# Kernel tuning notes

Measured on AMD Instinct MI355X. Metric: run time of the kernel, lower is better.

## Reference

```python
import jax, jax.numpy as jnp
import numpy as np


def setup_inputs() -> dict:
    key = jax.random.key(0)
    ks = jax.random.split(key, 6)
    L, B, A, I, H = 512, 64, 256, 256, 512
    scale = 1.0 / np.sqrt(H)
    return {
        "action_features": jax.random.normal(ks[0], (L, B, A), dtype=jnp.float32),
        "input_feature": jax.random.normal(ks[1], (B, I), dtype=jnp.float32),
        "h0": jnp.zeros((B, H), dtype=jnp.float32),
        "c0": jnp.zeros((B, H), dtype=jnp.float32),
        "W_ih": jax.random.normal(ks[2], (4 * H, I + A), dtype=jnp.float32) * scale,
        "W_hh": jax.random.normal(ks[3], (4 * H, H), dtype=jnp.float32) * scale,
        "b_ih": jax.random.normal(ks[4], (4 * H,), dtype=jnp.float32) * scale,
        "b_hh": jax.random.normal(ks[5], (4 * H,), dtype=jnp.float32) * scale,
    }


def reference(action_features, input_feature, h0, c0, W_ih, W_hh, b_ih, b_hh):
    # action_features: [L, B, A] (time-major); input_feature: [B, I]
    H = h0.shape[-1]
    L = action_features.shape[0]
    # Precompute the input-side projection for all timesteps at once:
    # x_t = concat([input_feature, a_t]) -> x_t @ W_ih.T + b_ih
    # Split W_ih into the input_feature part and the action part.
    I = input_feature.shape[-1]
    W_i, W_a = W_ih[:, :I], W_ih[:, I:]
    # [B, 4H] contribution from the static input_feature (same every step)
    static_gates = input_feature @ W_i.T + b_ih + b_hh
    # [L, B, 4H] contribution from the per-step action features
    act_gates = jnp.einsum("lba,ga->lbg", action_features, W_a)

    def step(carry, g_t):
        h, c = carry
        gates = g_t + static_gates + h @ W_hh.T  # [B, 4H]
        i, f, g, o = jnp.split(gates, 4, axis=-1)
        i = jax.nn.sigmoid(i)
        f = jax.nn.sigmoid(f)
        g = jnp.tanh(g)
        o = jax.nn.sigmoid(o)
        c_new = f * c + i * g
        h_new = o * jnp.tanh(c_new)
        return (h_new, c_new), h_new

    (h_n, c_n), hs = jax.lax.scan(step, (h0, c0), act_gates)
    return hs, h_n, c_n
```

## Files before the change

### kernel.cpp

```cpp
#include <hip/hip_runtime.h>
#include <hip/hip_bf16.h>


#define NWG     64
#define LSTEPS  512
#define BATCH   64
#define HDIM    512
#define ADIM    256
#define GDIM    2048
#define KTOT    768
#define LBH     (LSTEPS*BATCH*HDIM)

typedef __attribute__((ext_vector_type(4))) float f32x4;
typedef __attribute__((ext_vector_type(8))) short s16x8;

__device__ __forceinline__ unsigned short f2bf(float f){
  unsigned u = __builtin_bit_cast(unsigned, f);
  u = (u + 0x7fffu + ((u >> 16) & 1u)) >> 16;
  return (unsigned short)u;
}
__device__ __forceinline__ float sigm(float x){ return 1.f / (1.f + __expf(-x)); }
__device__ __forceinline__ float ftanh(float x){ return 1.f - 2.f / (__expf(2.f*x) + 1.f); }


__global__ void cvt_act(const float* __restrict__ in, unsigned short* __restrict__ ob, int n8){
  int i = blockIdx.x * blockDim.x + threadIdx.x;
  if (i >= n8) return;
  const float4* p = (const float4*)in + (size_t)i * 2;
  float4 a = p[0], b = p[1];
  int4 o;
  o.x = (int)((unsigned)f2bf(a.x) | ((unsigned)f2bf(a.y) << 16));
  o.y = (int)((unsigned)f2bf(a.z) | ((unsigned)f2bf(a.w) << 16));
  o.z = (int)((unsigned)f2bf(b.x) | ((unsigned)f2bf(b.y) << 16));
  o.w = (int)((unsigned)f2bf(b.z) | ((unsigned)f2bf(b.w) << 16));
  ((int4*)ob)[i] = o;
}

__global__ void static_gates_k(const float* __restrict__ inp, const float* __restrict__ Wih,
                               const float* __restrict__ bih, const float* __restrict__ bhh,
                               float* __restrict__ statg){
  int g = blockIdx.x;
  int b = threadIdx.x;
  const float4* w = (const float4*)(Wih + (size_t)g * 512);
  const float4* x = (const float4*)(inp + (size_t)b * 256);
  float acc = 0.f;
#pragma unroll 8
  for (int i = 0; i < 64; ++i){
    float4 wv = w[i], xv = x[i];
    acc += wv.x*xv.x + wv.y*xv.y + wv.z*xv.z + wv.w*xv.w;
  }
  statg[b*GDIM + g] = acc + bih[g] + bhh[g];
}

__global__ void init_h(const float* __restrict__ h0, unsigned int* __restrict__ hbuf32){
  int i = blockIdx.x * blockDim.x + threadIdx.x;
  if (i < BATCH*256){
    unsigned lo = f2bf(h0[2*i]), hi = f2bf(h0[2*i+1]);
    hbuf32[BATCH*256 + i] = lo | (hi << 16);
  }
}


__global__ __launch_bounds__(256, 1) void lstm_persistent(
    const unsigned short* __restrict__ act_bf,
    const float*          __restrict__ statg,
    const float*          __restrict__ Whh,
    const float*          __restrict__ Wih,
    const float*          __restrict__ c0,
    float*                __restrict__ out,
    unsigned int*         __restrict__ hbuf32,
    unsigned int*         __restrict__ done)
{
  __shared__ short Albuf[64 * KTOT];
  __shared__ float gbuf[64 * 36];

  const int tid  = threadIdx.x;
  const int wgk  = blockIdx.x;
  const int lane = tid & 63;
  const int wid  = tid >> 6;
  const int wm   = wid & 1;
  const int wn   = wid >> 1;
  const int kgrp = (lane >> 4) * 8;

  const int cl   = wn*16 + (lane & 15);
  const int grow = (cl >> 3)*512 + wgk*8 + (cl & 7);
  s16x8 bw[24];
#pragma unroll
  for (int kk = 0; kk < 16; ++kk){
    s16x8 v;
    const int kb = kk*32 + kgrp;
#pragma unroll
    for (int e = 0; e < 8; ++e)
      v[e] = (short)f2bf(Whh[(size_t)grow*512 + kb + e]);
    bw[kk] = v;
  }
#pragma unroll
  for (int kk = 16; kk < 24; ++kk){
    s16x8 v;
    const int kb = kk*32 + kgrp;
#pragma unroll
    for (int e = 0; e < 8; ++e)
      v[e] = (short)f2bf(Wih[(size_t)grow*512 + (kb - 256) + e]);
    bw[kk] = v;
  }

  const int b_cu = tid >> 2;
  const int u0   = (tid & 3) * 2;
  const int j0   = wgk*8 + u0;
  float stat2[2][4], cr[2];
#pragma unroll
  for (int pi = 0; pi < 2; ++pi){
    const int j = j0 + pi;
#pragma unroll
    for (int g4 = 0; g4 < 4; ++g4)
      stat2[pi][g4] = statg[b_cu*GDIM + g4*512 + j];
    cr[pi] = c0[b_cu*HDIM + j];
  }

  for (int t = 0; t < LSTEPS; ++t){
    {
      const unsigned short* asrc = act_bf + (size_t)t * (BATCH*ADIM);
#pragma unroll
      for (int it = 0; it < 8; ++it){
        const int idx = it*256 + tid;
        const int r = idx >> 5, ch = idx & 31;
        int4 v = *(const int4*)(asrc + r*ADIM + ch*8);
        *(int4*)(&Albuf[r*KTOT + 512 + ((ch ^ (r & 7)) * 8)]) = v;
      }
    }
    if (t > 0){
      while (__hip_atomic_load(&done[t-1], __ATOMIC_RELAXED, __HIP_MEMORY_SCOPE_AGENT) < NWG){}
      __builtin_amdgcn_fence(__ATOMIC_ACQUIRE, "agent");
    }
    {
      const int4* hp = (const int4*)(hbuf32 + ((t+1) & 1) * (BATCH*256));
#pragma unroll
      for (int it = 0; it < 16; ++it){
        const int idx = it*256 + tid;
        const int r = idx >> 6, ch = idx & 63;
        int4 v = hp[r*64 + ch];
        *(int4*)(&Albuf[r*KTOT + ((ch ^ (r & 7)) * 8)]) = v;
      }
    }
    __syncthreads();

    f32x4 acc[2];
#pragma unroll
    for (int m = 0; m < 2; ++m){
      f32x4 a = {0.f, 0.f, 0.f, 0.f};
      const int r  = wm*32 + m*16 + (lane & 15);
      const short* arow = &Albuf[r * KTOT];
      const int sw = (r & 7) * 8;
#pragma unroll
      for (int kk = 0; kk < 24; ++kk){
        const int col = (kk*32 + kgrp) ^ sw;
        s16x8 af = *(const s16x8*)(arow + col);
        a = __builtin_amdgcn_mfma_f32_16x16x32_bf16(af, bw[kk], a, 0, 0, 0);
      }
      acc[m] = a;
    }
#pragma unroll
    for (int m = 0; m < 2; ++m){
      const int base_b = wm*32 + m*16 + ((lane >> 4) * 4);
#pragma unroll
      for (int r4 = 0; r4 < 4; ++r4)
        gbuf[(base_b + r4)*36 + cl] = acc[m][r4];
    }
    __syncthreads();

    {
      const float* gb = &gbuf[b_cu*36];
      float hv[2];
#pragma unroll
      for (int pi = 0; pi < 2; ++pi){
        const int u = u0 + pi;
        float iv = gb[u]      + stat2[pi][0];
        float fv = gb[8 + u]  + stat2[pi][1];
        float gv = gb[16 + u] + stat2[pi][2];
        float ov = gb[24 + u] + stat2[pi][3];
        iv = sigm(iv); fv = sigm(fv); gv = ftanh(gv); ov = sigm(ov);
        float c = fv * cr[pi] + iv * gv;
        cr[pi] = c;
        hv[pi] = ov * ftanh(c);
      }
      float2 h2; h2.x = hv[0]; h2.y = hv[1];
      *(float2*)&out[((size_t)t*BATCH + b_cu)*HDIM + j0] = h2;
      unsigned pk = (unsigned)f2bf(hv[0]) | ((unsigned)f2bf(hv[1]) << 16);
      __hip_atomic_store(&hbuf32[(t & 1)*(BATCH*256) + b_cu*256 + (j0 >> 1)], pk,
                         __ATOMIC_RELAXED, __HIP_MEMORY_SCOPE_AGENT);
      if (t == LSTEPS-1){
        float2 c2; c2.x = cr[0]; c2.y = cr[1];
        *(float2*)&out[LBH + b_cu*HDIM + j0] = h2;
        *(float2*)&out[LBH + BATCH*HDIM + b_cu*HDIM + j0] = c2;
      }
    }
    __syncthreads();
    if (tid == 0)
      __hip_atomic_fetch_add(&done[t], 1u, __ATOMIC_RELAXED, __HIP_MEMORY_SCOPE_AGENT);
  }
}


extern "C" void kernel_launch(void* const* d_in, const int* in_sizes, int n_in,
                              void* d_out, int out_size, void* d_ws, size_t ws_size,
                              hipStream_t stream){
  const float* act = (const float*)d_in[0];
  const float* inp = (const float*)d_in[1];
  const float* h0  = (const float*)d_in[2];
  const float* c0  = (const float*)d_in[3];
  const float* Wih = (const float*)d_in[4];
  const float* Whh = (const float*)d_in[5];
  const float* bih = (const float*)d_in[6];
  const float* bhh = (const float*)d_in[7];
  float* out = (float*)d_out;

  char* ws = (char*)d_ws;
  unsigned short* act_bf = (unsigned short*)ws;
  unsigned int*   hbuf32 = (unsigned int*)(ws + 16777216);
  float*          statg  = (float*)(ws + 16777216 + 131072);
  unsigned int*   done   = (unsigned int*)(ws + 16777216 + 131072 + 524288);

  hipMemsetAsync(done, 0, LSTEPS * sizeof(unsigned int), stream);
  cvt_act<<<4096, 256, 0, stream>>>(act, act_bf, (LSTEPS*BATCH*ADIM)/8);
  static_gates_k<<<GDIM, 64, 0, stream>>>(inp, Wih, bih, bhh, statg);
  init_h<<<64, 256, 0, stream>>>(h0, hbuf32);
  lstm_persistent<<<NWG, 256, 0, stream>>>(act_bf, statg, Whh, Wih, c0, out, hbuf32, done);
}
```

Baseline: 2.428 ms.

## Restructure persistent LSTM step: weights as A operand, per-WG flags, prefetch actions

Swaps the MFMA operand roles so the weights sit in the A operand, arranged so that each lane's accumulator holds all four gates (i, f, g, o) for one hidden unit. The gate math can then run straight from registers, and the gbuf shared-memory round trip plus one barrier are gone. The grid barrier changes from an atomic counter fetch_add per step to per-workgroup flag stores in a ring of 8 slots, polled by a whole wavefront with __all. The next step's action tile is now loaded into LDS after the h publish, overlapping it with the wait, and h is published as 64-bit atomic stores by one wave. The risk is memory ordering: the acquire fence was removed and replaced with relaxed loads plus an s_waitcnt, and h values are read back from LDS after the barrier.

```diff
diff --git a/kernel.cpp b/kernel.cpp
--- a/kernel.cpp
+++ b/kernel.cpp
@@ -10,9 +10,11 @@
 #define GDIM    2048
 #define KTOT    768
 #define LBH     (LSTEPS*BATCH*HDIM)
+#define HWORDS  (BATCH*256)
 
 typedef __attribute__((ext_vector_type(4))) float f32x4;
 typedef __attribute__((ext_vector_type(8))) short s16x8;
+typedef unsigned long long u64t;
 
 __device__ __forceinline__ unsigned short f2bf(float f){
   unsigned u = __builtin_bit_cast(unsigned, f);
@@ -54,9 +56,9 @@
 
 __global__ void init_h(const float* __restrict__ h0, unsigned int* __restrict__ hbuf32){
   int i = blockIdx.x * blockDim.x + threadIdx.x;
-  if (i < BATCH*256){
+  if (i < HWORDS){
     unsigned lo = f2bf(h0[2*i]), hi = f2bf(h0[2*i+1]);
-    hbuf32[BATCH*256 + i] = lo | (hi << 16);
+    hbuf32[HWORDS + i] = lo | (hi << 16);
   }
 }
 
@@ -72,19 +74,19 @@
     unsigned int*         __restrict__ done)
 {
   __shared__ short Albuf[64 * KTOT];
-  __shared__ float gbuf[64 * 36];
-
-  const int tid  = threadIdx.x;
-  const int wgk  = blockIdx.x;
-  const int lane = tid & 63;
-  const int wid  = tid >> 6;
-  const int wm   = wid & 1;
-  const int wn   = wid >> 1;
-  const int kgrp = (lane >> 4) * 8;
-
-  const int cl   = wn*16 + (lane & 15);
-  const int grow = (cl >> 3)*512 + wgk*8 + (cl & 7);
-  s16x8 bw[24];
+  __shared__ float hb[64 * 9];
+
+  const int tid   = threadIdx.x;
+  const int wgk   = blockIdx.x;
+  const int lane  = tid & 63;
+  const int wid   = tid >> 6;
+  const int m     = wid & 1;
+  const int npair = wid >> 1;
+  const int kgrp  = (lane >> 4) * 8;
+
+  const int rit  = lane & 15;
+  const int grow = (rit & 3)*512 + wgk*8 + m*4 + (rit >> 2);
+  s16x8 aw[24];
 #pragma unroll
   for (int kk = 0; kk < 16; ++kk){
     s16x8 v;
@@ -92,7 +94,7 @@
 #pragma unroll
     for (int e = 0; e < 8; ++e)
       v[e] = (short)f2bf(Whh[(size_t)grow*512 + kb + e]);
-    bw[kk] = v;
+    aw[kk] = v;
   }
 #pragma unroll
   for (int kk = 16; kk < 24; ++kk){
@@ -101,25 +103,126 @@
 #pragma unroll
     for (int e = 0; e < 8; ++e)
       v[e] = (short)f2bf(Wih[(size_t)grow*512 + (kb - 256) + e]);
-    bw[kk] = v;
-  }
-
-  const int b_cu = tid >> 2;
-  const int u0   = (tid & 3) * 2;
-  const int j0   = wgk*8 + u0;
-  float stat2[2][4], cr[2];
-#pragma unroll
-  for (int pi = 0; pi < 2; ++pi){
-    const int j = j0 + pi;
-#pragma unroll
-    for (int g4 = 0; g4 < 4; ++g4)
-      stat2[pi][g4] = statg[b_cu*GDIM + g4*512 + j];
-    cr[pi] = c0[b_cu*HDIM + j];
+    aw[kk] = v;
+  }
+
+  const int bA = (npair*2)*16 + (lane & 15);
+  const int bB = bA + 16;
+  const int j  = wgk*8 + m*4 + (lane >> 4);
+  const int uloc = m*4 + (lane >> 4);
+  float stat[2][4], cr[2];
+#pragma unroll
+  for (int g4 = 0; g4 < 4; ++g4){
+    stat[0][g4] = statg[bA*GDIM + g4*512 + j];
+    stat[1][g4] = statg[bB*GDIM + g4*512 + j];
+  }
+  cr[0] = c0[bA*HDIM + j];
+  cr[1] = c0[bB*HDIM + j];
+
+  const int r0  = bA;
+  const int sw0 = (r0 & 7) * 8;
+
+  {
+    const unsigned short* asrc = act_bf;
+#pragma unroll
+    for (int it = 0; it < 8; ++it){
+      const int idx = it*256 + tid;
+      const int r = idx >> 5, ch = idx & 31;
+      int4 v = *(const int4*)(asrc + r*ADIM + ch*8);
+      *(int4*)(&Albuf[r*KTOT + 512 + ((ch ^ (r & 7)) * 8)]) = v;
+    }
   }
 
   for (int t = 0; t < LSTEPS; ++t){
-    {
-      const unsigned short* asrc = act_bf + (size_t)t * (BATCH*ADIM);
+    if (t > 0){
+      unsigned v;
+      const unsigned* fl = &done[((t-1) & 7)*64 + lane];
+      do {
+        v = __hip_atomic_load(fl, __ATOMIC_RELAXED, __HIP_MEMORY_SCOPE_AGENT);
+      } while (!__all(v == (unsigned)t));
+    }
+    {
+      const u64t* hsrc = (const u64t*)(hbuf32 + ((t+1) & 1) * HWORDS);
+#pragma unroll
+      for (int it = 0; it < 16; ++it){
+        const int idx = it*256 + tid;
+        const int r = idx >> 6, ch = idx & 63;
+        u64t a = __hip_atomic_load(hsrc + r*128 + ch*2,     __ATOMIC_RELAXED, __HIP_MEMORY_SCOPE_AGENT);
+        u64t b = __hip_atomic_load(hsrc + r*128 + ch*2 + 1, __ATOMIC_RELAXED, __HIP_MEMORY_SCOPE_AGENT);
+        int4 v;
+        v.x = (int)(unsigned)(a & 0xffffffffull);
+        v.y = (int)(unsigned)(a >> 32);
+        v.z = (int)(unsigned)(b & 0xffffffffull);
+        v.w = (int)(unsigned)(b >> 32);
+        *(int4*)(&Albuf[r*KTOT + ((ch ^ (r & 7)) * 8)]) = v;
+      }
+    }
+    __syncthreads();
+
+    f32x4 acc0 = {0.f,0.f,0.f,0.f}, acc1 = {0.f,0.f,0.f,0.f};
+    {
+      const short* arow0 = &Albuf[r0 * KTOT];
+      const short* arow1 = &Albuf[(r0+16) * KTOT];
+#pragma unroll
+      for (int kk = 0; kk < 24; ++kk){
+        const int col = (kk*32 + kgrp) ^ sw0;
+        s16x8 b0 = *(const s16x8*)(arow0 + col);
+        s16x8 b1 = *(const s16x8*)(arow1 + col);
+        acc0 = __builtin_amdgcn_mfma_f32_16x16x32_bf16(aw[kk], b0, acc0, 0, 0, 0);
+        acc1 = __builtin_amdgcn_mfma_f32_16x16x32_bf16(aw[kk], b1, acc1, 0, 0, 0);
+      }
+    }
+
+    float hv[2];
+    {
+      float iv = sigm(acc0[0] + stat[0][0]);
+      float fv = sigm(acc0[1] + stat[0][1]);
+      float gv = ftanh(acc0[2] + stat[0][2]);
+      float ov = sigm(acc0[3] + stat[0][3]);
+      float c = fv * cr[0] + iv * gv;
+      cr[0] = c; hv[0] = ov * ftanh(c);
+      iv = sigm(acc1[0] + stat[1][0]);
+      fv = sigm(acc1[1] + stat[1][1]);
+      gv = ftanh(acc1[2] + stat[1][2]);
+      ov = sigm(acc1[3] + stat[1][3]);
+      c = fv * cr[1] + iv * gv;
+      cr[1] = c; hv[1] = ov * ftanh(c);
+    }
+    hb[bA*9 + uloc] = hv[0];
+    hb[bB*9 + uloc] = hv[1];
+    __syncthreads();
+
+    if (tid < 64){
+      const int b = tid;
+      float h0 = hb[b*9+0], h1 = hb[b*9+1], h2 = hb[b*9+2], h3 = hb[b*9+3];
+      float h4 = hb[b*9+4], h5 = hb[b*9+5], h6 = hb[b*9+6], h7 = hb[b*9+7];
+      unsigned w0 = (unsigned)f2bf(h0) | ((unsigned)f2bf(h1) << 16);
+      unsigned w1 = (unsigned)f2bf(h2) | ((unsigned)f2bf(h3) << 16);
+      unsigned w2 = (unsigned)f2bf(h4) | ((unsigned)f2bf(h5) << 16);
+      unsigned w3 = (unsigned)f2bf(h6) | ((unsigned)f2bf(h7) << 16);
+      u64t lo = (u64t)w0 | ((u64t)w1 << 32);
+      u64t hi = (u64t)w2 | ((u64t)w3 << 32);
+      u64t* dst = (u64t*)(hbuf32 + (t & 1)*HWORDS + b*256 + wgk*4);
+      __hip_atomic_store(dst,     lo, __ATOMIC_RELAXED, __HIP_MEMORY_SCOPE_AGENT);
+      __hip_atomic_store(dst + 1, hi, __ATOMIC_RELAXED, __HIP_MEMORY_SCOPE_AGENT);
+    }
+    asm volatile("s_waitcnt vmcnt(0)" ::: "memory");
+    if (tid == 0)
+      __hip_atomic_store(&done[(t & 7)*64 + wgk], (unsigned)(t+1),
+                         __ATOMIC_RELAXED, __HIP_MEMORY_SCOPE_AGENT);
+
+    {
+      const int b = tid >> 2, q = (tid & 3)*2;
+      float2 h2o; h2o.x = hb[b*9+q]; h2o.y = hb[b*9+q+1];
+      *(float2*)&out[((size_t)t*BATCH + b)*HDIM + wgk*8 + q] = h2o;
+    }
+    if (t == LSTEPS-1){
+      out[LBH + bA*HDIM + j] = hv[0];
+      out[LBH + bB*HDIM + j] = hv[1];
+      out[LBH + BATCH*HDIM + bA*HDIM + j] = cr[0];
+      out[LBH + BATCH*HDIM + bB*HDIM + j] = cr[1];
+    } else {
+      const unsigned short* asrc = act_bf + (size_t)(t+1) * (BATCH*ADIM);
 #pragma unroll
       for (int it = 0; it < 8; ++it){
         const int idx = it*256 + tid;
@@ -128,75 +231,6 @@
         *(int4*)(&Albuf[r*KTOT + 512 + ((ch ^ (r & 7)) * 8)]) = v;
       }
     }
-    if (t > 0){
-      while (__hip_atomic_load(&done[t-1], __ATOMIC_RELAXED, __HIP_MEMORY_SCOPE_AGENT) < NWG){}
-      __builtin_amdgcn_fence(__ATOMIC_ACQUIRE, "agent");
-    }
-    {
-      const int4* hp = (const int4*)(hbuf32 + ((t+1) & 1) * (BATCH*256));
-#pragma unroll
-      for (int it = 0; it < 16; ++it){
-        const int idx = it*256 + tid;
-        const int r = idx >> 6, ch = idx & 63;
-        int4 v = hp[r*64 + ch];
-        *(int4*)(&Albuf[r*KTOT + ((ch ^ (r & 7)) * 8)]) = v;
-      }
-    }
-    __syncthreads();
-
-    f32x4 acc[2];
-#pragma unroll
-    for (int m = 0; m < 2; ++m){
-      f32x4 a = {0.f, 0.f, 0.f, 0.f};
-      const int r  = wm*32 + m*16 + (lane & 15);
-      const short* arow = &Albuf[r * KTOT];
-      const int sw = (r & 7) * 8;
-#pragma unroll
-      for (int kk = 0; kk < 24; ++kk){
-        const int col = (kk*32 + kgrp) ^ sw;
-        s16x8 af = *(const s16x8*)(arow + col);
-        a = __builtin_amdgcn_mfma_f32_16x16x32_bf16(af, bw[kk], a, 0, 0, 0);
-      }
-      acc[m] = a;
-    }
-#pragma unroll
-    for (int m = 0; m < 2; ++m){
-      const int base_b = wm*32 + m*16 + ((lane >> 4) * 4);
-#pragma unroll
-      for (int r4 = 0; r4 < 4; ++r4)
-        gbuf[(base_b + r4)*36 + cl] = acc[m][r4];
-    }
-    __syncthreads();
-
-    {
-      const float* gb = &gbuf[b_cu*36];
-      float hv[2];
-#pragma unroll
-      for (int pi = 0; pi < 2; ++pi){
-        const int u = u0 + pi;
-        float iv = gb[u]      + stat2[pi][0];
-        float fv = gb[8 + u]  + stat2[pi][1];
-        float gv = gb[16 + u] + stat2[pi][2];
-        float ov = gb[24 + u] + stat2[pi][3];
-        iv = sigm(iv); fv = sigm(fv); gv = ftanh(gv); ov = sigm(ov);
-        float c = fv * cr[pi] + iv * gv;
-        cr[pi] = c;
-        hv[pi] = ov * ftanh(c);
-      }
-      float2 h2; h2.x = hv[0]; h2.y = hv[1];
-      *(float2*)&out[((size_t)t*BATCH + b_cu)*HDIM + j0] = h2;
-      unsigned pk = (unsigned)f2bf(hv[0]) | ((unsigned)f2bf(hv[1]) << 16);
-      __hip_atomic_store(&hbuf32[(t & 1)*(BATCH*256) + b_cu*256 + (j0 >> 1)], pk,
-                         __ATOMIC_RELAXED, __HIP_MEMORY_SCOPE_AGENT);
-      if (t == LSTEPS-1){
-        float2 c2; c2.x = cr[0]; c2.y = cr[1];
-        *(float2*)&out[LBH + b_cu*HDIM + j0] = h2;
-        *(float2*)&out[LBH + BATCH*HDIM + b_cu*HDIM + j0] = c2;
-      }
-    }
-    __syncthreads();
-    if (tid == 0)
-      __hip_atomic_fetch_add(&done[t], 1u, __ATOMIC_RELAXED, __HIP_MEMORY_SCOPE_AGENT);
   }
 }
 
@@ -220,7 +254,7 @@
   float*          statg  = (float*)(ws + 16777216 + 131072);
   unsigned int*   done   = (unsigned int*)(ws + 16777216 + 131072 + 524288);
 
-  hipMemsetAsync(done, 0, LSTEPS * sizeof(unsigned int), stream);
+  hipMemsetAsync(done, 0, 8*64*sizeof(unsigned int), stream);
   cvt_act<<<4096, 256, 0, stream>>>(act, act_bf, (LSTEPS*BATCH*ADIM)/8);
   static_gates_k<<<GDIM, 64, 0, stream>>>(inp, Wih, bih, bhh, statg);
   init_h<<<64, 256, 0, stream>>>(h0, hbuf32);
```

After: 4.180 ms. +72.2%, slower.

## Replace atomic-counter barrier with per-block flags and prefetch next-step actions

Applied to the files above, without the earlier changes.

The grid barrier changes from a single shared atomic counter per step to per-workgroup flag slots in a ring of 8. Each waiting wave polls all 64 flags in parallel, one per lane, and checks them with a wave-wide all. The block signals completion right after publishing h, so the fp32 output writes and the next step's action tile load into LDS now happen after the signal and overlap with other blocks' wait. This removes atomic contention on one address and takes off-critical-path work out of the step latency. The risk is that overwriting the action region of LDS after the last sync relies on the next iteration's barrier ordering, and the ring of 8 assumes blocks never drift 8 steps apart.

```diff
diff --git a/kernel.cpp b/kernel.cpp
--- a/kernel.cpp
+++ b/kernel.cpp
@@ -10,6 +10,7 @@
 #define GDIM    2048
 #define KTOT    768
 #define LBH     (LSTEPS*BATCH*HDIM)
+#define HWORDS  (BATCH*256)
 
 typedef __attribute__((ext_vector_type(4))) float f32x4;
 typedef __attribute__((ext_vector_type(8))) short s16x8;
@@ -54,9 +55,9 @@
 
 __global__ void init_h(const float* __restrict__ h0, unsigned int* __restrict__ hbuf32){
   int i = blockIdx.x * blockDim.x + threadIdx.x;
-  if (i < BATCH*256){
+  if (i < HWORDS){
     unsigned lo = f2bf(h0[2*i]), hi = f2bf(h0[2*i+1]);
-    hbuf32[BATCH*256 + i] = lo | (hi << 16);
+    hbuf32[HWORDS + i] = lo | (hi << 16);
   }
 }
 
@@ -117,23 +118,28 @@
     cr[pi] = c0[b_cu*HDIM + j];
   }
 
+  {
+    const unsigned short* asrc = act_bf;
+#pragma unroll
+    for (int it = 0; it < 8; ++it){
+      const int idx = it*256 + tid;
+      const int r = idx >> 5, ch = idx & 31;
+      int4 v = *(const int4*)(asrc + r*ADIM + ch*8);
+      *(int4*)(&Albuf[r*KTOT + 512 + ((ch ^ (r & 7)) * 8)]) = v;
+    }
+  }
+
   for (int t = 0; t < LSTEPS; ++t){
+    if (t > 0){
+      unsigned v;
+      const unsigned* fl = &done[((t-1) & 7)*64 + lane];
+      do {
+        v = __hip_atomic_load(fl, __ATOMIC_RELAXED, __HIP_MEMORY_SCOPE_AGENT);
+      } while (!__all(v == (unsigned)t));
+      __builtin_amdgcn_fence(__ATOMIC_ACQUIRE, "agent");
+    }
     {
-      const unsigned short* asrc = act_bf + (size_t)t * (BATCH*ADIM);
-#pragma unroll
-      for (int it = 0; it < 8; ++it){
-        const int idx = it*256 + tid;
-        const int r = idx >> 5, ch = idx & 31;
-        int4 v = *(const int4*)(asrc + r*ADIM + ch*8);
-        *(int4*)(&Albuf[r*KTOT + 512 + ((ch ^ (r & 7)) * 8)]) = v;
-      }
-    }
-    if (t > 0){
-      while (__hip_atomic_load(&done[t-1], __ATOMIC_RELAXED, __HIP_MEMORY_SCOPE_AGENT) < NWG){}
-      __builtin_amdgcn_fence(__ATOMIC_ACQUIRE, "agent");
-    }
-    {
-      const int4* hp = (const int4*)(hbuf32 + ((t+1) & 1) * (BATCH*256));
+      const int4* hp = (const int4*)(hbuf32 + ((t+1) & 1) * HWORDS);
 #pragma unroll
       for (int it = 0; it < 16; ++it){
         const int idx = it*256 + tid;
@@ -168,9 +174,9 @@
     }
     __syncthreads();
 
+    float hv[2];
     {
       const float* gb = &gbuf[b_cu*36];
-      float hv[2];
 #pragma unroll
       for (int pi = 0; pi < 2; ++pi){
         const int u = u0 + pi;
@@ -183,20 +189,34 @@
         cr[pi] = c;
         hv[pi] = ov * ftanh(c);
       }
-      float2 h2; h2.x = hv[0]; h2.y = hv[1];
-      *(float2*)&out[((size_t)t*BATCH + b_cu)*HDIM + j0] = h2;
       unsigned pk = (unsigned)f2bf(hv[0]) | ((unsigned)f2bf(hv[1]) << 16);
-      __hip_atomic_store(&hbuf32[(t & 1)*(BATCH*256) + b_cu*256 + (j0 >> 1)], pk,
+      __hip_atomic_store(&hbuf32[(t & 1)*HWORDS + b_cu*256 + (j0 >> 1)], pk,
                          __ATOMIC_RELAXED, __HIP_MEMORY_SCOPE_AGENT);
-      if (t == LSTEPS-1){
-        float2 c2; c2.x = cr[0]; c2.y = cr[1];
-        *(float2*)&out[LBH + b_cu*HDIM + j0] = h2;
-        *(float2*)&out[LBH + BATCH*HDIM + b_cu*HDIM + j0] = c2;
-      }
     }
     __syncthreads();
     if (tid == 0)
-      __hip_atomic_fetch_add(&done[t], 1u, __ATOMIC_RELAXED, __HIP_MEMORY_SCOPE_AGENT);
+      __hip_atomic_store(&done[(t & 7)*64 + wgk], (unsigned)(t+1),
+                         __ATOMIC_RELAXED, __HIP_MEMORY_SCOPE_AGENT);
+
+    {
+      float2 h2o; h2o.x = hv[0]; h2o.y = hv[1];
+      *(float2*)&out[((size_t)t*BATCH + b_cu)*HDIM + j0] = h2o;
+    }
+    if (t == LSTEPS-1){
+      float2 c2o; c2o.x = cr[0]; c2o.y = cr[1];
+      float2 h2o; h2o.x = hv[0]; h2o.y = hv[1];
+      *(float2*)&out[LBH + b_cu*HDIM + j0] = h2o;
+      *(float2*)&out[LBH + BATCH*HDIM + b_cu*HDIM + j0] = c2o;
+    } else {
+      const unsigned short* asrc = act_bf + (size_t)(t+1) * (BATCH*ADIM);
+#pragma unroll
+      for (int it = 0; it < 8; ++it){
+        const int idx = it*256 + tid;
+        const int r = idx >> 5, ch = idx & 31;
+        int4 v = *(const int4*)(asrc + r*ADIM + ch*8);
+        *(int4*)(&Albuf[r*KTOT + 512 + ((ch ^ (r & 7)) * 8)]) = v;
+      }
+    }
   }
 }
 
@@ -220,7 +240,7 @@
   float*          statg  = (float*)(ws + 16777216 + 131072);
   unsigned int*   done   = (unsigned int*)(ws + 16777216 + 131072 + 524288);
 
-  hipMemsetAsync(done, 0, LSTEPS * sizeof(unsigned int), stream);
+  hipMemsetAsync(done, 0, 8*64*sizeof(unsigned int), stream);
   cvt_act<<<4096, 256, 0, stream>>>(act, act_bf, (LSTEPS*BATCH*ADIM)/8);
   static_gates_k<<<GDIM, 64, 0, stream>>>(inp, Wih, bih, bhh, statg);
   init_h<<<64, 256, 0, stream>>>(h0, hbuf32);
```

New measurement: 4.180 ms. 72.2% more time.
